# Optimization experiments

Measured on AMD Instinct MI355X. Metric: run time of the kernel, lower is better.

Reference implementation:

```python
import math
import jax, jax.numpy as jnp
import numpy as np

N_HEADS = 8
EPS = 1e-6


def setup_inputs() -> dict:
    key = jax.random.key(0)
    k0, k1, k2, k3, k4 = jax.random.split(key, 5)
    B, T, E = 2, 1024, 512
    s = 1.0 / math.sqrt(E)
    x = jax.random.normal(k0, (B, T, E), dtype=jnp.float32)
    w_qkv = jax.random.normal(k1, (3 * E, E), dtype=jnp.float32) * s
    b_qkv = jax.random.normal(k2, (3 * E,), dtype=jnp.float32) * s
    w_out = jax.random.normal(k3, (E, E), dtype=jnp.float32) * s
    b_out = jax.random.normal(k4, (E,), dtype=jnp.float32) * s
    return {"x": x, "w_qkv": w_qkv, "b_qkv": b_qkv, "w_out": w_out, "b_out": b_out}


def reference(x, w_qkv, b_qkv, w_out, b_out):
    B, T, C = x.shape
    H = N_HEADS
    d = C // H

    qkv = x @ w_qkv.T + b_qkv                      # [B,T,3C]
    q, k, v = jnp.split(qkv, 3, axis=-1)

    def to_heads(t):
        return t.reshape(B, T, H, d).transpose(0, 2, 1, 3).astype(jnp.float32)  # [B,H,T,d]

    q, k, v = to_heads(q), to_heads(k), to_heads(v)

    pos = jnp.arange(T, dtype=jnp.float32)
    ang = (math.pi / 2) * pos / T
    cos_w = jnp.cos(ang)[None, None, :, None]      # [1,1,T,1]
    sin_w = jnp.sin(ang)[None, None, :, None]

    q_prime = jax.nn.relu(q)
    k_prime = jax.nn.relu(k)
    q_cos, q_sin = q_prime * cos_w, q_prime * sin_w
    k_cos, k_sin = k_prime * cos_w, k_prime * sin_w

    # causal linear attention via cumulative outer products (cosFormer)
    kv_cos_cs = jnp.cumsum(jnp.einsum('bhtd,bhte->bhtde', k_cos, v), axis=2)
    context = jnp.einsum('bhtd,bhtde->bhte', q_cos, kv_cos_cs)
    kv_sin_cs = jnp.cumsum(jnp.einsum('bhtd,bhte->bhtde', k_sin, v), axis=2)
    context = context + jnp.einsum('bhtd,bhtde->bhte', q_sin, kv_sin_cs)

    norm = (jnp.einsum('bhtd,bhtd->bht', q_cos, jnp.cumsum(k_cos, axis=2))
            + jnp.einsum('bhtd,bhtd->bht', q_sin, jnp.cumsum(k_sin, axis=2)))
    out = context / (norm[..., None] + EPS)        # [B,H,T,d]

    out = out.astype(x.dtype).transpose(0, 2, 1, 3).reshape(B, T, C)
    return out @ w_out.T + b_out
```

## Files before the change

kernel.cpp:

```cpp
#include <hip/hip_runtime.h>

typedef __bf16 bf16_t;
typedef __bf16 bf16x4 __attribute__((ext_vector_type(4)));
typedef __bf16 bf16x8 __attribute__((ext_vector_type(8)));
typedef float f32x4 __attribute__((ext_vector_type(4)));

#define T_SEQ 1024
#define EMB   512
#define NH    8
#define HD    64
#define BATCH 2
#define NBH   (BATCH*NH)
#define CHUNK 64
#define NCHUNK (T_SEQ/CHUNK)
#define NBLK  (NBH*NCHUNK)
#define LDA   72


__global__ __launch_bounds__(256) void cvt_kernel(
    const float* __restrict__ src, bf16_t* __restrict__ dst, int n4)
{
    int i = blockIdx.x * 256 + threadIdx.x;
    if (i < n4) {
        float4 v = ((const float4*)src)[i];
        bf16x4 o;
        o[0] = (bf16_t)v.x; o[1] = (bf16_t)v.y;
        o[2] = (bf16_t)v.z; o[3] = (bf16_t)v.w;
        ((bf16x4*)dst)[i] = o;
    }
}

__global__ __launch_bounds__(256) void qkv_gemm_kernel(
    const bf16_t* __restrict__ X, const bf16_t* __restrict__ W,
    const float* __restrict__ bias,
    bf16_t* __restrict__ qq, bf16_t* __restrict__ kk, bf16_t* __restrict__ vv)
{
    const int w = threadIdx.x >> 6;
    const int lane = threadIdx.x & 63;
    const int rsel = lane & 15;
    const int koff = (lane >> 4) * 8;
    const int m0 = blockIdx.x * 128 + (w & 1) * 64;
    const int n0 = blockIdx.y * 128 + (w >> 1) * 64;
    f32x4 acc[4][4] = {};
    const bf16_t* Ap = X + (m0 + rsel) * EMB + koff;
    const bf16_t* Bp = W + (n0 + rsel) * EMB + koff;
#pragma unroll 2
    for (int k0 = 0; k0 < EMB; k0 += 32) {
        bf16x8 af[4], bfr[4];
        for (int i = 0; i < 4; ++i)
            af[i] = *(const bf16x8*)(Ap + i * 16 * EMB + k0);
        for (int j = 0; j < 4; ++j)
            bfr[j] = *(const bf16x8*)(Bp + j * 16 * EMB + k0);
        for (int i = 0; i < 4; ++i)
            for (int j = 0; j < 4; ++j)
                acc[i][j] = __builtin_amdgcn_mfma_f32_16x16x32_bf16(
                    af[i], bfr[j], acc[i][j], 0, 0, 0);
    }
    for (int j = 0; j < 4; ++j) {
        const int n = n0 + j * 16 + rsel;
        const float bn = bias[n];
        const int sec = n >> 9;
        const int c = n & 511;
        const int h = c >> 6, e = c & 63;
        for (int i = 0; i < 4; ++i) {
            const int mb = m0 + i * 16 + (lane >> 4) * 4;
            for (int r = 0; r < 4; ++r) {
                int m = mb + r;
                int b = m >> 10, t = m & 1023;
                float val = acc[i][j][r] + bn;
                int di = ((b * NH + h) * T_SEQ + t) * HD + e;
                if (sec == 0) {
                    qq[di] = (bf16_t)fmaxf(val, 0.f);
                } else if (sec == 1) {
                    kk[di] = (bf16_t)fmaxf(val, 0.f);
                } else {
                    vv[di] = (bf16_t)val;
                }
            }
        }
    }
}

__global__ __launch_bounds__(256) void chunk_sum_kernel(
    const bf16_t* __restrict__ kk, const bf16_t* __restrict__ vv,
    bf16_t* __restrict__ Ssc, bf16_t* __restrict__ Sss,
    float* __restrict__ zc, float* __restrict__ zs)
{
    const int blk = blockIdx.x;
    const int ch = blk & 15;
    __shared__ __align__(16) bf16_t sk[CHUNK * HD];
    __shared__ __align__(16) bf16_t sv[CHUNK * HD];
    __shared__ float cwt[CHUNK], swt[CHUNK];
    const int base = blk * CHUNK * HD;
    for (int i = threadIdx.x; i < CHUNK * HD / 8; i += 256) {
        ((uint4*)sk)[i] = ((const uint4*)(kk + base))[i];
        ((uint4*)sv)[i] = ((const uint4*)(vv + base))[i];
    }
    if (threadIdx.x < CHUNK) {
        int tg = ch * CHUNK + threadIdx.x;
        float ang = 1.5707963267948966f * (float)tg * (1.0f / (float)T_SEQ);
        cwt[threadIdx.x] = cosf(ang);
        swt[threadIdx.x] = sinf(ang);
    }
    __syncthreads();
    const int i  = threadIdx.x & 63;
    const int jg = (threadIdx.x >> 6) * 16;
    float ac[16], as[16];
    for (int jj = 0; jj < 16; ++jj) { ac[jj] = 0.f; as[jj] = 0.f; }
    for (int t = 0; t < CHUNK; ++t) {
        float kv = (float)sk[t * HD + i];
        float kc_ = kv * cwt[t];
        float ks_ = kv * swt[t];
        for (int jj = 0; jj < 16; ++jj) {
            float vj = (float)sv[t * HD + jg + jj];
            ac[jj] += kc_ * vj;
            as[jj] += ks_ * vj;
        }
    }
    bf16_t* oc = Ssc + blk * HD * HD;
    bf16_t* os = Sss + blk * HD * HD;
    for (int jj = 0; jj < 16; ++jj) {
        oc[(jg + jj) * HD + i] = (bf16_t)ac[jj];
        os[(jg + jj) * HD + i] = (bf16_t)as[jj];
    }
    if (threadIdx.x < HD) {
        int ii = threadIdx.x;
        float s = 0.f;
        for (int t = 0; t < CHUNK; ++t) s += (float)sk[t * HD + ii] * cwt[t];
        zc[blk * HD + ii] = s;
    } else if (threadIdx.x < 2 * HD) {
        int ii = threadIdx.x - HD;
        float s = 0.f;
        for (int t = 0; t < CHUNK; ++t) s += (float)sk[t * HD + ii] * swt[t];
        zs[blk * HD + ii] = s;
    }
}

__global__ __launch_bounds__(256) void scan_kernel(
    bf16_t* __restrict__ Ssc, bf16_t* __restrict__ Sss,
    float* __restrict__ zc, float* __restrict__ zs)
{
    const int bh = blockIdx.x;
    for (int e = threadIdx.x; e < HD * HD; e += 256) {
        float r1 = 0.f, r2 = 0.f;
        for (int c = 0; c < NCHUNK; ++c) {
            int idx = (bh * NCHUNK + c) * HD * HD + e;
            float t1 = (float)Ssc[idx]; Ssc[idx] = (bf16_t)r1; r1 += t1;
            float t2 = (float)Sss[idx]; Sss[idx] = (bf16_t)r2; r2 += t2;
        }
    }
    if (threadIdx.x < HD) {
        int e = threadIdx.x;
        float r1 = 0.f, r2 = 0.f;
        for (int c = 0; c < NCHUNK; ++c) {
            int idx = (bh * NCHUNK + c) * HD + e;
            float t1 = zc[idx]; zc[idx] = r1; r1 += t1;
            float t2 = zs[idx]; zs[idx] = r2; r2 += t2;
        }
    }
}

__global__ __launch_bounds__(256) void chunk_out_kernel(
    const bf16_t* __restrict__ qq, const bf16_t* __restrict__ kk,
    const bf16_t* __restrict__ vv,
    const bf16_t* __restrict__ SscT, const bf16_t* __restrict__ SssT,
    const float* __restrict__ zc, const float* __restrict__ zs,
    bf16_t* __restrict__ Y)
{
    const int blk = blockIdx.x;
    const int bh = blk >> 4, ch = blk & 15;
    __shared__ __align__(16) bf16_t sq [CHUNK * LDA];
    __shared__ __align__(16) bf16_t sk [CHUNK * LDA];
    __shared__ __align__(16) bf16_t svT[CHUNK * LDA];
    __shared__ __align__(16) bf16_t sct[CHUNK * LDA];
    __shared__ __align__(16) bf16_t sst[CHUNK * LDA];
    __shared__ __align__(16) bf16_t sp [CHUNK * LDA];
    __shared__ float cwt[CHUNK], swt[CHUNK], cosd[CHUNK];
    __shared__ float zcl[CHUNK], zsl[CHUNK], nrm[CHUNK];

    const int base = blk * CHUNK * HD;
    for (int i = threadIdx.x; i < CHUNK * HD / 8; i += 256) {
        int row = i >> 3, g = i & 7;
        ((uint4*)(sq + row * LDA))[g]  = ((const uint4*)(qq + base))[i];
        ((uint4*)(sk + row * LDA))[g]  = ((const uint4*)(kk + base))[i];
        ((uint4*)(sct + row * LDA))[g] = ((const uint4*)(SscT + base))[i];
        ((uint4*)(sst + row * LDA))[g] = ((const uint4*)(SssT + base))[i];
        bf16x8 v8 = *(const bf16x8*)(vv + base + i * 8);
        int t = i >> 3, e0 = (i & 7) * 8;
        for (int j = 0; j < 8; ++j) svT[(e0 + j) * LDA + t] = v8[j];
    }
    if (threadIdx.x < CHUNK) {
        int tl = threadIdx.x;
        int tg = ch * CHUNK + tl;
        float angg = 1.5707963267948966f * (float)tg * (1.0f / (float)T_SEQ);
        cwt[tl] = cosf(angg);
        swt[tl] = sinf(angg);
        cosd[tl] = cosf(1.5707963267948966f * (float)tl * (1.0f / (float)T_SEQ));
        zcl[tl] = zc[blk * HD + tl];
        zsl[tl] = zs[blk * HD + tl];
    }
    __syncthreads();

    const int w = threadIdx.x >> 6;
    const int lane = threadIdx.x & 63;
    const int rsel = lane & 15;
    const int koff = (lane >> 4) * 8;
    const int myrow = w * 16 + rsel;

    bf16x8 aq0 = *(const bf16x8*)(sq + myrow * LDA + koff);
    bf16x8 aq1 = *(const bf16x8*)(sq + myrow * LDA + koff + 32);
    for (int nt = 0; nt < 4; ++nt) {
        const int n0 = nt * 16;
        f32x4 pacc = {0.f, 0.f, 0.f, 0.f};
        bf16x8 b0 = *(const bf16x8*)(sk + (n0 + rsel) * LDA + koff);
        bf16x8 b1 = *(const bf16x8*)(sk + (n0 + rsel) * LDA + koff + 32);
        pacc = __builtin_amdgcn_mfma_f32_16x16x32_bf16(aq0, b0, pacc, 0, 0, 0);
        pacc = __builtin_amdgcn_mfma_f32_16x16x32_bf16(aq1, b1, pacc, 0, 0, 0);
        const int s = n0 + (lane & 15);
        const int tb = w * 16 + (lane >> 4) * 4;
        for (int r = 0; r < 4; ++r) {
            int t = tb + r;
            float p = (s <= t) ? pacc[r] * cosd[t - s] : 0.f;
            sp[t * LDA + s] = (bf16_t)p;
        }
    }

    if (lane < 16) {
        int row = w * 16 + lane;
        float nv = 0.f;
        const bf16x8* pr = (const bf16x8*)(sp + row * LDA);
        for (int g = 0; g < 8; ++g) {
            bf16x8 pv = pr[g];
            for (int j = 0; j < 8; ++j) nv += (float)pv[j];
        }
        float cwr = cwt[row], swr = swt[row];
        const bf16x8* qr = (const bf16x8*)(sq + row * LDA);
        for (int g = 0; g < 8; ++g) {
            bf16x8 qv = qr[g];
            for (int j = 0; j < 8; ++j)
                nv += (float)qv[j] * (cwr * zcl[g * 8 + j] + swr * zsl[g * 8 + j]);
        }
        nrm[row] = nv;
    }

    const float cwq = cwt[myrow], swq = swt[myrow];
    bf16x8 qc0, qc1, qs0, qs1;
    for (int j = 0; j < 8; ++j) {
        qc0[j] = (bf16_t)((float)aq0[j] * cwq);
        qc1[j] = (bf16_t)((float)aq1[j] * cwq);
        qs0[j] = (bf16_t)((float)aq0[j] * swq);
        qs1[j] = (bf16_t)((float)aq1[j] * swq);
    }
    bf16x8 ap0 = *(const bf16x8*)(sp + myrow * LDA + koff);
    bf16x8 ap1 = *(const bf16x8*)(sp + myrow * LDA + koff + 32);

    const int b = bh >> 3, h = bh & 7;
    for (int nt = 0; nt < 4; ++nt) {
        const int n0 = nt * 16;
        const bf16_t* bvp = svT + (n0 + rsel) * LDA + koff;
        const bf16_t* bcp = sct + (n0 + rsel) * LDA + koff;
        const bf16_t* bsp = sst + (n0 + rsel) * LDA + koff;
        f32x4 acc = {0.f, 0.f, 0.f, 0.f};
        acc = __builtin_amdgcn_mfma_f32_16x16x32_bf16(ap0, *(const bf16x8*)(bvp), acc, 0, 0, 0);
        acc = __builtin_amdgcn_mfma_f32_16x16x32_bf16(ap1, *(const bf16x8*)(bvp + 32), acc, 0, 0, 0);
        acc = __builtin_amdgcn_mfma_f32_16x16x32_bf16(qc0, *(const bf16x8*)(bcp), acc, 0, 0, 0);
        acc = __builtin_amdgcn_mfma_f32_16x16x32_bf16(qc1, *(const bf16x8*)(bcp + 32), acc, 0, 0, 0);
        acc = __builtin_amdgcn_mfma_f32_16x16x32_bf16(qs0, *(const bf16x8*)(bsp), acc, 0, 0, 0);
        acc = __builtin_amdgcn_mfma_f32_16x16x32_bf16(qs1, *(const bf16x8*)(bsp + 32), acc, 0, 0, 0);
        const int col = n0 + (lane & 15);
        const int tb = w * 16 + (lane >> 4) * 4;
        for (int r = 0; r < 4; ++r) {
            int row = tb + r;
            float inv = 1.0f / (nrm[row] + 1e-6f);
            int tg = ch * CHUNK + row;
            Y[((b * T_SEQ + tg) * EMB) + h * HD + col] = (bf16_t)(acc[r] * inv);
        }
    }
}

__global__ __launch_bounds__(256) void out_gemm_kernel(
    const bf16_t* __restrict__ Yb, const bf16_t* __restrict__ W,
    const float* __restrict__ bias, float* __restrict__ out)
{
    const int w = threadIdx.x >> 6;
    const int lane = threadIdx.x & 63;
    const int rsel = lane & 15;
    const int koff = (lane >> 4) * 8;
    const int m0 = blockIdx.x * 64 + (w & 1) * 32;
    const int n0 = blockIdx.y * 64 + (w >> 1) * 32;
    f32x4 acc[2][2] = {};
    const bf16_t* Ap = Yb + (m0 + rsel) * EMB + koff;
    const bf16_t* Bp = W + (n0 + rsel) * EMB + koff;
#pragma unroll 2
    for (int k0 = 0; k0 < EMB; k0 += 32) {
        bf16x8 af[2], bfr[2];
        for (int i = 0; i < 2; ++i)
            af[i] = *(const bf16x8*)(Ap + i * 16 * EMB + k0);
        for (int j = 0; j < 2; ++j)
            bfr[j] = *(const bf16x8*)(Bp + j * 16 * EMB + k0);
        for (int i = 0; i < 2; ++i)
            for (int j = 0; j < 2; ++j)
                acc[i][j] = __builtin_amdgcn_mfma_f32_16x16x32_bf16(
                    af[i], bfr[j], acc[i][j], 0, 0, 0);
    }
    for (int j = 0; j < 2; ++j) {
        const int n = n0 + j * 16 + rsel;
        const float bn = bias[n];
        for (int i = 0; i < 2; ++i) {
            const int mb = m0 + i * 16 + (lane >> 4) * 4;
            for (int r = 0; r < 4; ++r)
                out[(mb + r) * EMB + n] = acc[i][j][r] + bn;
        }
    }
}

extern "C" void kernel_launch(void* const* d_in, const int* in_sizes, int n_in,
                              void* d_out, int out_size, void* d_ws, size_t ws_size,
                              hipStream_t stream) {
    const float* x     = (const float*)d_in[0];
    const float* w_qkv = (const float*)d_in[1];
    const float* b_qkv = (const float*)d_in[2];
    const float* w_out = (const float*)d_in[3];
    const float* b_out = (const float*)d_in[4];
    float* out = (float*)d_out;

    char* w = (char*)d_ws;
    const size_t N_X   = (size_t)BATCH * T_SEQ * EMB;
    const size_t N_WQ  = (size_t)3 * EMB * EMB;
    const size_t N_WO  = (size_t)EMB * EMB;
    bf16_t* xb   = (bf16_t*)w;                 w += N_X  * sizeof(bf16_t);
    bf16_t* wqb  = (bf16_t*)w;                 w += N_WQ * sizeof(bf16_t);
    bf16_t* wob  = (bf16_t*)w;                 w += N_WO * sizeof(bf16_t);
    const size_t SZ_BHTD = (size_t)NBH * T_SEQ * HD * sizeof(bf16_t);
    bf16_t* qq = (bf16_t*)w;                   w += SZ_BHTD;
    bf16_t* kk = (bf16_t*)w;                   w += SZ_BHTD;
    bf16_t* vv = (bf16_t*)w;                   w += SZ_BHTD;
    bf16_t* Y  = (bf16_t*)w;                   w += SZ_BHTD;
    bf16_t* Ssc = (bf16_t*)w;                  w += (size_t)NBLK * HD * HD * sizeof(bf16_t);
    bf16_t* Sss = (bf16_t*)w;                  w += (size_t)NBLK * HD * HD * sizeof(bf16_t);
    float* zc = (float*)w;                     w += (size_t)NBLK * HD * sizeof(float);
    float* zs = (float*)w;

    cvt_kernel<<<(int)(N_X / 4 + 255) / 256, 256, 0, stream>>>(x, xb, (int)(N_X / 4));
    cvt_kernel<<<(int)(N_WQ / 4 + 255) / 256, 256, 0, stream>>>(w_qkv, wqb, (int)(N_WQ / 4));
    cvt_kernel<<<(int)(N_WO / 4 + 255) / 256, 256, 0, stream>>>(w_out, wob, (int)(N_WO / 4));

    qkv_gemm_kernel<<<dim3(2048 / 128, 1536 / 128), 256, 0, stream>>>(
        xb, wqb, b_qkv, qq, kk, vv);
    chunk_sum_kernel<<<NBLK, 256, 0, stream>>>(kk, vv, Ssc, Sss, zc, zs);
    scan_kernel<<<NBH, 256, 0, stream>>>(Ssc, Sss, zc, zs);
    chunk_out_kernel<<<NBLK, 256, 0, stream>>>(qq, kk, vv, Ssc, Sss, zc, zs, Y);
    out_gemm_kernel<<<dim3(2048 / 64, 512 / 64), 256, 0, stream>>>(
        Y, wob, b_out, out);
}
```

Before: 139.2 us.

## Fold chunk-state prefix scan into chunk_out and merge conversion launches

Removes the separate scan kernel, which ran with only 16 blocks and walked 16 chunks serially. Each chunk_out block now sums the preceding chunks' state matrices and normalizer vectors itself, straight into shared memory. The three float-to-bf16 conversion launches become one kernel, and the out GEMM unroll factor goes from 2 to 4. In exchange, later chunks do redundant prefix reads (up to 15 states each), and the total state traffic grows roughly quadratically in chunk count.

```diff
diff --git a/kernel.cpp b/kernel.cpp
--- a/kernel.cpp
+++ b/kernel.cpp
@@ -17,17 +17,21 @@
 #define LDA   72
 
 
-__global__ __launch_bounds__(256) void cvt_kernel(
-    const float* __restrict__ src, bf16_t* __restrict__ dst, int n4)
+__global__ __launch_bounds__(256) void cvt3_kernel(
+    const float* __restrict__ x, const float* __restrict__ wq,
+    const float* __restrict__ wo,
+    bf16_t* __restrict__ xb, bf16_t* __restrict__ wqb, bf16_t* __restrict__ wob)
 {
     int i = blockIdx.x * 256 + threadIdx.x;
-    if (i < n4) {
-        float4 v = ((const float4*)src)[i];
-        bf16x4 o;
-        o[0] = (bf16_t)v.x; o[1] = (bf16_t)v.y;
-        o[2] = (bf16_t)v.z; o[3] = (bf16_t)v.w;
-        ((bf16x4*)dst)[i] = o;
-    }
+    const float* s; bf16_t* d; int off;
+    if (i < 262144)      { s = x;  d = xb;  off = i; }
+    else if (i < 458752) { s = wq; d = wqb; off = i - 262144; }
+    else                 { s = wo; d = wob; off = i - 458752; }
+    float4 v = ((const float4*)s)[off];
+    bf16x4 o;
+    o[0] = (bf16_t)v.x; o[1] = (bf16_t)v.y;
+    o[2] = (bf16_t)v.z; o[3] = (bf16_t)v.w;
+    ((bf16x4*)d)[off] = o;
 }
 
 __global__ __launch_bounds__(256) void qkv_gemm_kernel(
@@ -136,30 +140,6 @@
     }
 }
 
-__global__ __launch_bounds__(256) void scan_kernel(
-    bf16_t* __restrict__ Ssc, bf16_t* __restrict__ Sss,
-    float* __restrict__ zc, float* __restrict__ zs)
-{
-    const int bh = blockIdx.x;
-    for (int e = threadIdx.x; e < HD * HD; e += 256) {
-        float r1 = 0.f, r2 = 0.f;
-        for (int c = 0; c < NCHUNK; ++c) {
-            int idx = (bh * NCHUNK + c) * HD * HD + e;
-            float t1 = (float)Ssc[idx]; Ssc[idx] = (bf16_t)r1; r1 += t1;
-            float t2 = (float)Sss[idx]; Sss[idx] = (bf16_t)r2; r2 += t2;
-        }
-    }
-    if (threadIdx.x < HD) {
-        int e = threadIdx.x;
-        float r1 = 0.f, r2 = 0.f;
-        for (int c = 0; c < NCHUNK; ++c) {
-            int idx = (bh * NCHUNK + c) * HD + e;
-            float t1 = zc[idx]; zc[idx] = r1; r1 += t1;
-            float t2 = zs[idx]; zs[idx] = r2; r2 += t2;
-        }
-    }
-}
-
 __global__ __launch_bounds__(256) void chunk_out_kernel(
     const bf16_t* __restrict__ qq, const bf16_t* __restrict__ kk,
     const bf16_t* __restrict__ vv,
@@ -183,21 +163,50 @@
         int row = i >> 3, g = i & 7;
         ((uint4*)(sq + row * LDA))[g]  = ((const uint4*)(qq + base))[i];
         ((uint4*)(sk + row * LDA))[g]  = ((const uint4*)(kk + base))[i];
-        ((uint4*)(sct + row * LDA))[g] = ((const uint4*)(SscT + base))[i];
-        ((uint4*)(sst + row * LDA))[g] = ((const uint4*)(SssT + base))[i];
         bf16x8 v8 = *(const bf16x8*)(vv + base + i * 8);
         int t = i >> 3, e0 = (i & 7) * 8;
         for (int j = 0; j < 8; ++j) svT[(e0 + j) * LDA + t] = v8[j];
     }
-    if (threadIdx.x < CHUNK) {
+    {
+        const int e0 = threadIdx.x * 16;
+        float accC[16], accS[16];
+        for (int j = 0; j < 16; ++j) { accC[j] = 0.f; accS[j] = 0.f; }
+        const int sb = bh * NCHUNK * HD * HD + e0;
+        for (int c = 0; c < ch; ++c) {
+            const bf16x8* pc = (const bf16x8*)(SscT + sb + c * HD * HD);
+            const bf16x8* ps = (const bf16x8*)(SssT + sb + c * HD * HD);
+            bf16x8 c0 = pc[0], c1 = pc[1], s0 = ps[0], s1 = ps[1];
+            for (int j = 0; j < 8; ++j) {
+                accC[j] += (float)c0[j];  accC[8 + j] += (float)c1[j];
+                accS[j] += (float)s0[j];  accS[8 + j] += (float)s1[j];
+            }
+        }
+        const int row = threadIdx.x >> 2, col = (threadIdx.x & 3) * 16;
+        bf16x8 oc0, oc1, os0, os1;
+        for (int j = 0; j < 8; ++j) {
+            oc0[j] = (bf16_t)accC[j];  oc1[j] = (bf16_t)accC[8 + j];
+            os0[j] = (bf16_t)accS[j];  os1[j] = (bf16_t)accS[8 + j];
+        }
+        *(bf16x8*)(sct + row * LDA + col) = oc0;
+        *(bf16x8*)(sct + row * LDA + col + 8) = oc1;
+        *(bf16x8*)(sst + row * LDA + col) = os0;
+        *(bf16x8*)(sst + row * LDA + col + 8) = os1;
+    }
+    if (threadIdx.x < HD) {
         int tl = threadIdx.x;
+        float s = 0.f;
+        for (int c = 0; c < ch; ++c) s += zc[(bh * NCHUNK + c) * HD + tl];
+        zcl[tl] = s;
         int tg = ch * CHUNK + tl;
         float angg = 1.5707963267948966f * (float)tg * (1.0f / (float)T_SEQ);
         cwt[tl] = cosf(angg);
         swt[tl] = sinf(angg);
         cosd[tl] = cosf(1.5707963267948966f * (float)tl * (1.0f / (float)T_SEQ));
-        zcl[tl] = zc[blk * HD + tl];
-        zsl[tl] = zs[blk * HD + tl];
+    } else if (threadIdx.x < 2 * HD) {
+        int i = threadIdx.x - HD;
+        float s = 0.f;
+        for (int c = 0; c < ch; ++c) s += zs[(bh * NCHUNK + c) * HD + i];
+        zsl[i] = s;
     }
     __syncthreads();
 
@@ -291,7 +300,7 @@
     f32x4 acc[2][2] = {};
     const bf16_t* Ap = Yb + (m0 + rsel) * EMB + koff;
     const bf16_t* Bp = W + (n0 + rsel) * EMB + koff;
-#pragma unroll 2
+#pragma unroll 4
     for (int k0 = 0; k0 < EMB; k0 += 32) {
         bf16x8 af[2], bfr[2];
         for (int i = 0; i < 2; ++i)
@@ -336,20 +345,16 @@
     bf16_t* kk = (bf16_t*)w;                   w += SZ_BHTD;
     bf16_t* vv = (bf16_t*)w;                   w += SZ_BHTD;
     bf16_t* Y  = (bf16_t*)w;                   w += SZ_BHTD;
-    bf16_t* Ssc = (bf16_t*)w;                  w += (size_t)NBLK * HD * HD * sizeof(bf16_t);
-    bf16_t* Sss = (bf16_t*)w;                  w += (size_t)NBLK * HD * HD * sizeof(bf16_t);
+    bf16_t* SscT = (bf16_t*)w;                 w += (size_t)NBLK * HD * HD * sizeof(bf16_t);
+    bf16_t* SssT = (bf16_t*)w;                 w += (size_t)NBLK * HD * HD * sizeof(bf16_t);
     float* zc = (float*)w;                     w += (size_t)NBLK * HD * sizeof(float);
     float* zs = (float*)w;
 
-    cvt_kernel<<<(int)(N_X / 4 + 255) / 256, 256, 0, stream>>>(x, xb, (int)(N_X / 4));
-    cvt_kernel<<<(int)(N_WQ / 4 + 255) / 256, 256, 0, stream>>>(w_qkv, wqb, (int)(N_WQ / 4));
-    cvt_kernel<<<(int)(N_WO / 4 + 255) / 256, 256, 0, stream>>>(w_out, wob, (int)(N_WO / 4));
-
+    cvt3_kernel<<<2048, 256, 0, stream>>>(x, w_qkv, w_out, xb, wqb, wob);
     qkv_gemm_kernel<<<dim3(2048 / 128, 1536 / 128), 256, 0, stream>>>(
         xb, wqb, b_qkv, qq, kk, vv);
-    chunk_sum_kernel<<<NBLK, 256, 0, stream>>>(kk, vv, Ssc, Sss, zc, zs);
-    scan_kernel<<<NBH, 256, 0, stream>>>(Ssc, Sss, zc, zs);
-    chunk_out_kernel<<<NBLK, 256, 0, stream>>>(qq, kk, vv, Ssc, Sss, zc, zs, Y);
+    chunk_sum_kernel<<<NBLK, 256, 0, stream>>>(kk, vv, SscT, SssT, zc, zs);
+    chunk_out_kernel<<<NBLK, 256, 0, stream>>>(qq, kk, vv, SscT, SssT, zc, zs, Y);
     out_gemm_kernel<<<dim3(2048 / 64, 512 / 64), 256, 0, stream>>>(
         Y, wob, b_out, out);
 }
```

Measured after the change: 126.7 us. 1.1x faster.
